# Kernel optimization log

Hardware: AMD Instinct MI355X
Metric: run time of the kernel (lower is better)

## Reference

```python
import jax, jax.numpy as jnp
import numpy as np

B, S, H, DH = 2, 2048, 16, 64
D = H * DH


def setup_inputs() -> dict:
    key = jax.random.key(0)
    ks = jax.random.split(key, 10)
    std = 0.02
    return {
        "hidden_states": jax.random.normal(ks[0], (B, S, D), jnp.float32),
        "mask": jax.random.randint(ks[1], (B, S), 0, 2, jnp.int64 if jax.config.jax_enable_x64 else jnp.int32),
        "Wq": jax.random.normal(ks[2], (D, D), jnp.float32) * std,
        "bq": jnp.zeros((D,), jnp.float32),
        "Wk": jax.random.normal(ks[3], (D, D), jnp.float32) * std,
        "bk": jnp.zeros((D,), jnp.float32),
        "Wv": jax.random.normal(ks[4], (D, D), jnp.float32) * std,
        "bv": jnp.zeros((D,), jnp.float32),
        "Wo": jax.random.normal(ks[5], (D, D), jnp.float32) * std,
        "bo": jnp.zeros((D,), jnp.float32),
    }


def _split_heads(x):
    # (B, S, H*DH) -> (B, H, S, DH)
    b, s, _ = x.shape
    return x.reshape(b, s, H, DH).transpose(0, 2, 1, 3)


def reference(hidden_states, mask, Wq, bq, Wk, bk, Wv, bv, Wo, bo):
    # Linear projections (torch nn.Linear: x @ W.T + b)
    q = _split_heads(hidden_states @ Wq.T + bq)
    k = _split_heads(hidden_states @ Wk.T + bk)
    v = _split_heads(hidden_states @ Wv.T + bv)

    scale = 1.0 / np.sqrt(DH).astype(np.float32)
    scores = jnp.einsum("bhqd,bhkd->bhqk", q, k) * scale  # (B,H,S,S)
    # mask out padded key positions (mask==0 -> -inf), broadcast over heads/queries
    scores = jnp.where(mask[:, None, None, :] == 0, -jnp.inf, scores)
    weights = jax.nn.softmax(scores, axis=-1)

    attended = jnp.einsum("bhqk,bhkd->bhqd", weights, v)  # (B,H,S,DH)
    merged = attended.transpose(0, 2, 1, 3).reshape(hidden_states.shape)  # (B,S,D)
    return merged @ Wo.T + bo
```

## Files before the change

### kernel.cpp

```cpp
#include <hip/hip_runtime.h>
#include <hip/hip_bf16.h>

typedef __bf16 bf16;
typedef __bf16 bf16x4 __attribute__((ext_vector_type(4)));
typedef __bf16 bf16x8 __attribute__((ext_vector_type(8)));
typedef float f32x4 __attribute__((ext_vector_type(4)));

#define B_ 2
#define S_ 2048
#define H_ 16
#define DH_ 64
#define D_ 1024
#define NT_ 4096

#define WAIT_VMCNT0() asm volatile("s_waitcnt vmcnt(0)" ::: "memory")
#define WAIT_LGKM0()  asm volatile("s_waitcnt lgkmcnt(0)" ::: "memory")

__device__ __forceinline__ void gld_lds16(const bf16* g, bf16* l) {
    __builtin_amdgcn_global_load_lds(
        (__attribute__((address_space(1))) void*)g,
        (__attribute__((address_space(3))) void*)l, 16, 0, 0);
}

__device__ __forceinline__ bf16 f2bf(float x) {
    union { float f; unsigned u; } v; v.f = x;
    unsigned short h = (unsigned short)((v.u + 0x7FFF + ((v.u >> 16) & 1)) >> 16);
    return __builtin_bit_cast(bf16, h);
}

__global__ __launch_bounds__(256) void cvt_kernel(
    const float* __restrict__ hs,
    const float* __restrict__ Wq, const float* __restrict__ Wk,
    const float* __restrict__ Wv, const float* __restrict__ Wo,
    bf16* __restrict__ hsb, bf16* __restrict__ wqkv, bf16* __restrict__ wob)
{
    int i = (blockIdx.x * 256 + threadIdx.x) * 4;
    const float* src;
    bf16* dst;
    if (i < 4194304) {
        src = hs + i; dst = hsb + i;
    } else if (i < 7340032) {
        int off = i - 4194304;
        int which = off >> 20;
        int within = off & 1048575;
        src = (which == 0 ? Wq : which == 1 ? Wk : Wv) + within;
        dst = wqkv + off;
    } else {
        int off = i - 7340032;
        src = Wo + off; dst = wob + off;
    }
    float4 v = *(const float4*)src;
    bf16x4 o = { (bf16)v.x, (bf16)v.y, (bf16)v.z, (bf16)v.w };
    *(bf16x4*)dst = o;
}

__global__ __launch_bounds__(256, 2) void gemm_bt(
    const bf16* __restrict__ A, const bf16* __restrict__ Bm,
    int mode,
    const float* __restrict__ b0, const float* __restrict__ b1,
    const float* __restrict__ b2,
    bf16* __restrict__ Qo, bf16* __restrict__ Ko, bf16* __restrict__ Vt,
    float* __restrict__ Co)
{
    const int K = 1024;
    __shared__ __attribute__((aligned(16))) bf16 sA[128 * 32];
    __shared__ __attribute__((aligned(16))) bf16 sB[128 * 32];

    int tid = threadIdx.x;
    int wave = tid >> 6, lane = tid & 63;
    int quad = lane >> 4, l16 = lane & 15;
    int m0 = blockIdx.x * 128;
    int n0 = blockIdx.y * 128;
    int wm = (wave & 1) * 64, wn = (wave >> 1) * 64;
    int fs = (l16 >> 1) & 3;

    f32x4 acc[4][4];
#pragma unroll
    for (int i = 0; i < 4; i++)
#pragma unroll
        for (int j = 0; j < 4; j++) acc[i][j] = (f32x4){0.f, 0.f, 0.f, 0.f};

    for (int k0 = 0; k0 < K; k0 += 32) {
#pragma unroll
        for (int i = 0; i < 2; i++) {
            int chunk = tid + i * 256;
            int row = chunk >> 2;
            int kc = ((chunk & 3) ^ ((row >> 1) & 3)) * 8;
            gld_lds16(A + (size_t)(m0 + row) * K + k0 + kc, &sA[chunk * 8]);
            gld_lds16(Bm + (size_t)(n0 + row) * K + k0 + kc, &sB[chunk * 8]);
        }
        WAIT_VMCNT0();
        __syncthreads();

        bf16x8 af[4], bfr[4];
#pragma unroll
        for (int i = 0; i < 4; i++)
            af[i] = *(const bf16x8*)&sA[(wm + i * 16 + l16) * 32 + (quad ^ fs) * 8];
#pragma unroll
        for (int j = 0; j < 4; j++)
            bfr[j] = *(const bf16x8*)&sB[(wn + j * 16 + l16) * 32 + (quad ^ fs) * 8];
#pragma unroll
        for (int i = 0; i < 4; i++)
#pragma unroll
            for (int j = 0; j < 4; j++)
                acc[i][j] = __builtin_amdgcn_mfma_f32_16x16x32_bf16(
                    af[i], bfr[j], acc[i][j], 0, 0, 0);
        __syncthreads();
    }

    if (mode == 0) {
        const float QSCALE = 0.125f * 1.44269504088896340736f;
#pragma unroll
        for (int j = 0; j < 4; j++) {
            int n = n0 + wn + j * 16 + l16;
            int region = n >> 10;
            int nn = n & 1023;
            int h = nn >> 6, d = nn & 63;
            float bias = (region == 0 ? b0 : region == 1 ? b1 : b2)[nn];
#pragma unroll
            for (int i = 0; i < 4; i++)
#pragma unroll
                for (int r = 0; r < 4; r++) {
                    int m = m0 + wm + i * 16 + quad * 4 + r;
                    int b = m >> 11, s = m & 2047;
                    int bh = b * H_ + h;
                    float v = acc[i][j][r] + bias;
                    if (region == 0)
                        Qo[((size_t)bh * S_ + s) * DH_ + d] = f2bf(v * QSCALE);
                    else if (region == 1)
                        Ko[((size_t)bh * S_ + s) * DH_ + d] = f2bf(v);
                    else
                        Vt[((size_t)bh * DH_ + d) * S_ + s] = f2bf(v);
                }
        }
    } else {
#pragma unroll
        for (int j = 0; j < 4; j++) {
            int n = n0 + wn + j * 16 + l16;
            float bias = b0[n];
#pragma unroll
            for (int i = 0; i < 4; i++)
#pragma unroll
                for (int r = 0; r < 4; r++) {
                    int m = m0 + wm + i * 16 + quad * 4 + r;
                    Co[(size_t)m * D_ + n] = acc[i][j][r] + bias;
                }
        }
    }
}

__global__ __launch_bounds__(256, 2) void attn_kernel(
    const bf16* __restrict__ Q, const bf16* __restrict__ Kg,
    const bf16* __restrict__ Vt, const int* __restrict__ mask,
    bf16* __restrict__ Og)
{
    __shared__ __attribute__((aligned(16))) bf16 sK[128 * 64];
    __shared__ __attribute__((aligned(16))) bf16 sV[64 * 128];
    __shared__ __attribute__((aligned(16))) bf16 sP[4][64 * 32];
    __shared__ float sMaddAll[S_];
    __shared__ float sPsumR[128];
    __shared__ float sPsumF[128];

    int tid = threadIdx.x;
    int wave = tid >> 6, lane = tid & 63;
    int quad = lane >> 4, l16 = lane & 15;
    int bh = blockIdx.y;
    int b = bh >> 4;
    int q0 = blockIdx.x * 128;
    int f8 = l16 & 7;
    int qh = wave & 1;
    int kh = wave >> 1;
    int X = (l16 & 6) ^ ((l16 & 8) >> 2);

    const bf16* Qb = Q + (size_t)bh * S_ * DH_;
    const bf16* Kb = Kg + (size_t)bh * S_ * DH_;
    const bf16* Vb = Vt + (size_t)bh * DH_ * S_;

#pragma unroll
    for (int i = 0; i < S_ / 256; i++) {
        int idx = tid + i * 256;
        sMaddAll[idx] = mask[b * S_ + idx] ? 0.f : -1e30f;
    }

    bf16x8 aq[4][2];
#pragma unroll
    for (int qt = 0; qt < 4; qt++) {
        int qrow = q0 + qh * 64 + qt * 16 + l16;
        aq[qt][0] = *(const bf16x8*)&Qb[(size_t)qrow * DH_ + quad * 8];
        aq[qt][1] = *(const bf16x8*)&Qb[(size_t)qrow * DH_ + 32 + quad * 8];
    }

    f32x4 o[4][4];
#pragma unroll
    for (int i = 0; i < 4; i++)
#pragma unroll
        for (int j = 0; j < 4; j++) o[i][j] = (f32x4){0.f, 0.f, 0.f, 0.f};
    float psum[4] = {0.f, 0.f, 0.f, 0.f};

    for (int kt = 0; kt < S_; kt += 128) {
#pragma unroll
        for (int i = 0; i < 8; i++) {
            int c = tid + i * 256;
            if (c < 1024) {
                int row = c >> 3;
                int g = (c & 7) ^ (row & 7);
                gld_lds16(&Kb[(size_t)(kt + row) * DH_ + g * 8], &sK[c * 8]);
            } else {
                int cv = c - 1024;
                int row = cv >> 4;
                int g = (cv & 15) ^ (row & 15);
                gld_lds16(&Vb[(size_t)row * S_ + kt + g * 8], &sV[cv * 8]);
            }
        }
        WAIT_VMCNT0();
        __syncthreads();

#pragma unroll
        for (int pass = 0; pass < 2; pass++) {
#pragma unroll
            for (int mtl = 0; mtl < 2; mtl++) {
                int keyrow = kh * 64 + pass * 32 + mtl * 16;
                bf16x8 ak0 = *(const bf16x8*)&sK[(keyrow + l16) * 64 + (quad ^ f8) * 8];
                bf16x8 ak1 = *(const bf16x8*)&sK[(keyrow + l16) * 64 + ((quad + 4) ^ f8) * 8];
                float4 ma4 = *(const float4*)&sMaddAll[kt + keyrow + quad * 4];
#pragma unroll
                for (int qt = 0; qt < 4; qt++) {
                    f32x4 c = (f32x4){0.f, 0.f, 0.f, 0.f};
                    c = __builtin_amdgcn_mfma_f32_16x16x32_bf16(ak0, aq[qt][0], c, 0, 0, 0);
                    c = __builtin_amdgcn_mfma_f32_16x16x32_bf16(ak1, aq[qt][1], c, 0, 0, 0);
                    float p0 = __builtin_amdgcn_exp2f(c[0] + ma4.x);
                    float p1 = __builtin_amdgcn_exp2f(c[1] + ma4.y);
                    float p2 = __builtin_amdgcn_exp2f(c[2] + ma4.z);
                    float p3 = __builtin_amdgcn_exp2f(c[3] + ma4.w);
                    psum[qt] += (p0 + p1) + (p2 + p3);
                    bf16x4 pk = { f2bf(p0), f2bf(p1), f2bf(p2), f2bf(p3) };
                    int g = (mtl * 4 + quad) ^ X;
                    *(bf16x4*)&sP[wave][(qt * 16 + l16) * 32 + g * 4] = pk;
                }
            }

            WAIT_LGKM0();
            bf16x8 ap[4];
#pragma unroll
            for (int qt = 0; qt < 4; qt++)
                ap[qt] = *(const bf16x8*)&sP[wave][(qt * 16 + l16) * 32 + ((quad * 2) ^ X) * 4];
#pragma unroll
            for (int dt = 0; dt < 4; dt++) {
                int g = (kh * 8 + pass * 4 + quad) ^ l16;
                bf16x8 bv = *(const bf16x8*)&sV[(dt * 16 + l16) * 128 + g * 8];
#pragma unroll
                for (int qt = 0; qt < 4; qt++)
                    o[qt][dt] = __builtin_amdgcn_mfma_f32_16x16x32_bf16(ap[qt], bv, o[qt][dt], 0, 0, 0);
            }
        }
        __syncthreads();
    }

#pragma unroll
    for (int qt = 0; qt < 4; qt++) {
        float v = psum[qt];
        v += __shfl_xor(v, 16);
        v += __shfl_xor(v, 32);
        psum[qt] = v;
    }

    __syncthreads();
    float* sRed = (wave == 2) ? (float*)sK : (float*)sV;
    if (wave >= 2) {
#pragma unroll
        for (int qt = 0; qt < 4; qt++)
#pragma unroll
            for (int dt = 0; dt < 4; dt++)
                *(f32x4*)&sRed[((qt * 4 + dt) * 64 + lane) * 4] = o[qt][dt];
#pragma unroll
        for (int qt = 0; qt < 4; qt++)
            sPsumR[(wave - 2) * 64 + qt * 16 + l16] = psum[qt];
    }
    __syncthreads();
    if (wave < 2) {
        float* src = (wave == 0) ? (float*)sK : (float*)sV;
#pragma unroll
        for (int qt = 0; qt < 4; qt++)
#pragma unroll
            for (int dt = 0; dt < 4; dt++)
                o[qt][dt] += *(const f32x4*)&src[((qt * 4 + dt) * 64 + lane) * 4];
#pragma unroll
        for (int qt = 0; qt < 4; qt++) {
            float v = psum[qt] + sPsumR[wave * 64 + qt * 16 + l16];
            sPsumF[wave * 64 + qt * 16 + l16] = v;
        }
        WAIT_LGKM0();
        int h = bh & 15;
#pragma unroll
        for (int qt = 0; qt < 4; qt++) {
            float4 ps = *(const float4*)&sPsumF[wave * 64 + qt * 16 + quad * 4];
            float rcp[4] = { 1.f / ps.x, 1.f / ps.y, 1.f / ps.z, 1.f / ps.w };
#pragma unroll
            for (int r = 0; r < 4; r++) {
                int s = q0 + qh * 64 + qt * 16 + quad * 4 + r;
#pragma unroll
                for (int dt = 0; dt < 4; dt++) {
                    int d = dt * 16 + l16;
                    Og[((size_t)(b * S_ + s)) * D_ + h * 64 + d] = f2bf(o[qt][dt][r] * rcp[r]);
                }
            }
        }
    }
}

extern "C" void kernel_launch(void* const* d_in, const int* in_sizes, int n_in,
                              void* d_out, int out_size, void* d_ws, size_t ws_size,
                              hipStream_t stream) {
    const float* hs = (const float*)d_in[0];
    const int* mask = (const int*)d_in[1];
    const float* Wq = (const float*)d_in[2];
    const float* bq = (const float*)d_in[3];
    const float* Wk = (const float*)d_in[4];
    const float* bk = (const float*)d_in[5];
    const float* Wv = (const float*)d_in[6];
    const float* bv = (const float*)d_in[7];
    const float* Wo = (const float*)d_in[8];
    const float* bo = (const float*)d_in[9];
    float* out = (float*)d_out;

    char* ws = (char*)d_ws;
    bf16* hsb  = (bf16*)(ws);
    bf16* wqkv = (bf16*)(ws + ((size_t)8 << 20));
    bf16* wob  = (bf16*)(ws + ((size_t)14 << 20));
    bf16* Qw   = (bf16*)(ws + ((size_t)16 << 20));
    bf16* Kw   = (bf16*)(ws + ((size_t)24 << 20));
    bf16* Vtw  = (bf16*)(ws + ((size_t)32 << 20));
    bf16* attn = (bf16*)(ws + ((size_t)40 << 20));

    cvt_kernel<<<8192, 256, 0, stream>>>(hs, Wq, Wk, Wv, Wo, hsb, wqkv, wob);
    gemm_bt<<<dim3(32, 24), 256, 0, stream>>>(hsb, wqkv, 0, bq, bk, bv,
                                              Qw, Kw, Vtw, nullptr);
    attn_kernel<<<dim3(16, 32), 256, 0, stream>>>(Qw, Kw, Vtw, mask, attn);
    gemm_bt<<<dim3(32, 8), 256, 0, stream>>>(attn, wob, 1, bo, nullptr, nullptr,
                                             nullptr, nullptr, nullptr, out);
}
```

Before: 205.9 us.

## Write V row-major from QKV GEMM and transpose in separate kernel

The QKV GEMM epilogue now writes V in the same row-major layout as Q and K instead of scattering strided transposed stores. A new LDS-based transpose kernel with XOR swizzling produces the transposed V that attention consumes, reusing the hidden-state workspace region. The attention P buffer switches from an XOR swizzle to row padding (stride 40), and the GEMM launch bound asks for 3 blocks per CU. This trades uncoalesced epilogue stores for an extra kernel launch and one extra read/write pass over V.

```diff
diff --git a/kernel.cpp b/kernel.cpp
--- a/kernel.cpp
+++ b/kernel.cpp
@@ -54,12 +54,12 @@
     *(bf16x4*)dst = o;
 }
 
-__global__ __launch_bounds__(256, 2) void gemm_bt(
+__global__ __launch_bounds__(256, 3) void gemm_bt(
     const bf16* __restrict__ A, const bf16* __restrict__ Bm,
     int mode,
     const float* __restrict__ b0, const float* __restrict__ b1,
     const float* __restrict__ b2,
-    bf16* __restrict__ Qo, bf16* __restrict__ Ko, bf16* __restrict__ Vt,
+    bf16* __restrict__ Qo, bf16* __restrict__ Ko, bf16* __restrict__ Vo,
     float* __restrict__ Co)
 {
     const int K = 1024;
@@ -130,7 +130,7 @@
                     else if (region == 1)
                         Ko[((size_t)bh * S_ + s) * DH_ + d] = f2bf(v);
                     else
-                        Vt[((size_t)bh * DH_ + d) * S_ + s] = f2bf(v);
+                        Vo[((size_t)bh * S_ + s) * DH_ + d] = f2bf(v);
                 }
         }
     } else {
@@ -146,6 +146,37 @@
                     Co[(size_t)m * D_ + n] = acc[i][j][r] + bias;
                 }
         }
+    }
+}
+
+__global__ __launch_bounds__(256) void transpose_v(
+    const bf16* __restrict__ V, bf16* __restrict__ Vt)
+{
+    __shared__ bf16 sT[64 * 64];
+    int tid = threadIdx.x;
+    int bh = blockIdx.y;
+    int st = blockIdx.x * 64;
+    const bf16* Vb = V + ((size_t)bh * S_ + st) * DH_;
+    bf16* Vo = Vt + (size_t)bh * DH_ * S_ + st;
+
+#pragma unroll
+    for (int i = 0; i < 2; i++) {
+        int c = tid + i * 256;
+        int s = c >> 3, dg = (c & 7) * 8;
+        bf16x8 v = *(const bf16x8*)&Vb[(size_t)s * DH_ + dg];
+        int g = dg >> 3;
+#pragma unroll
+        for (int j = 0; j < 8; j++)
+            sT[(dg + j) * 64 + (s ^ (g * 8))] = v[j];
+    }
+    __syncthreads();
+#pragma unroll
+    for (int i = 0; i < 2; i++) {
+        int c = tid + i * 256;
+        int d = c >> 3, sgq = c & 7;
+        int gg = d >> 3;
+        bf16x8 v = *(const bf16x8*)&sT[d * 64 + ((sgq ^ gg) * 8)];
+        *(bf16x8*)&Vo[(size_t)d * S_ + sgq * 8] = v;
     }
 }
 
@@ -156,7 +187,7 @@
 {
     __shared__ __attribute__((aligned(16))) bf16 sK[128 * 64];
     __shared__ __attribute__((aligned(16))) bf16 sV[64 * 128];
-    __shared__ __attribute__((aligned(16))) bf16 sP[4][64 * 32];
+    __shared__ __attribute__((aligned(16))) bf16 sP[4][64 * 40];
     __shared__ float sMaddAll[S_];
     __shared__ float sPsumR[128];
     __shared__ float sPsumF[128];
@@ -170,7 +201,6 @@
     int f8 = l16 & 7;
     int qh = wave & 1;
     int kh = wave >> 1;
-    int X = (l16 & 6) ^ ((l16 & 8) >> 2);
 
     const bf16* Qb = Q + (size_t)bh * S_ * DH_;
     const bf16* Kb = Kg + (size_t)bh * S_ * DH_;
@@ -234,8 +264,7 @@
                     float p3 = __builtin_amdgcn_exp2f(c[3] + ma4.w);
                     psum[qt] += (p0 + p1) + (p2 + p3);
                     bf16x4 pk = { f2bf(p0), f2bf(p1), f2bf(p2), f2bf(p3) };
-                    int g = (mtl * 4 + quad) ^ X;
-                    *(bf16x4*)&sP[wave][(qt * 16 + l16) * 32 + g * 4] = pk;
+                    *(bf16x4*)&sP[wave][(qt * 16 + l16) * 40 + (mtl * 4 + quad) * 4] = pk;
                 }
             }
 
@@ -243,7 +272,7 @@
             bf16x8 ap[4];
 #pragma unroll
             for (int qt = 0; qt < 4; qt++)
-                ap[qt] = *(const bf16x8*)&sP[wave][(qt * 16 + l16) * 32 + ((quad * 2) ^ X) * 4];
+                ap[qt] = *(const bf16x8*)&sP[wave][(qt * 16 + l16) * 40 + quad * 8];
 #pragma unroll
             for (int dt = 0; dt < 4; dt++) {
                 int g = (kh * 8 + pass * 4 + quad) ^ l16;
@@ -329,12 +358,14 @@
     bf16* wob  = (bf16*)(ws + ((size_t)14 << 20));
     bf16* Qw   = (bf16*)(ws + ((size_t)16 << 20));
     bf16* Kw   = (bf16*)(ws + ((size_t)24 << 20));
-    bf16* Vtw  = (bf16*)(ws + ((size_t)32 << 20));
+    bf16* Vw   = (bf16*)(ws + ((size_t)32 << 20));
     bf16* attn = (bf16*)(ws + ((size_t)40 << 20));
+    bf16* Vtw  = (bf16*)(ws);
 
     cvt_kernel<<<8192, 256, 0, stream>>>(hs, Wq, Wk, Wv, Wo, hsb, wqkv, wob);
     gemm_bt<<<dim3(32, 24), 256, 0, stream>>>(hsb, wqkv, 0, bq, bk, bv,
-                                              Qw, Kw, Vtw, nullptr);
+                                              Qw, Kw, Vw, nullptr);
+    transpose_v<<<dim3(32, 32), 256, 0, stream>>>(Vw, Vtw);
     attn_kernel<<<dim3(16, 32), 256, 0, stream>>>(Qw, Kw, Vtw, mask, attn);
     gemm_bt<<<dim3(32, 8), 256, 0, stream>>>(attn, wob, 1, bo, nullptr, nullptr,
                                              nullptr, nullptr, nullptr, out);
```

After: 208.8 us. About the same (+1.4%).
